# Kernel tuning notes

Measured on AMD Instinct MI355X. Metric: run time of the kernel, lower is better.

The kernel has to match this reference:

```python
import jax, jax.numpy as jnp
import numpy as np

DIM = 1024
HEADS = 16
HEAD_DIM = DIM // HEADS
SCALE = DIM ** -0.5  # note: original uses full dim, not head_dim


def setup_inputs() -> dict:
    key = jax.random.key(0)
    k1, k2, k3, k4 = jax.random.split(key, 4)
    x = jax.random.normal(k1, (4, 2048, DIM), dtype=jnp.float32)
    # nn.Linear(dim, 3*dim, bias=False): weight [3*dim, dim]; y = x @ W.T
    w_qkv = jax.random.normal(k2, (3 * DIM, DIM), dtype=jnp.float32) * (DIM ** -0.5)
    w_out = jax.random.normal(k3, (DIM, DIM), dtype=jnp.float32) * (DIM ** -0.5)
    b_out = jax.random.normal(k4, (DIM,), dtype=jnp.float32) * 0.01
    return {"x": x, "w_qkv": w_qkv, "w_out": w_out, "b_out": b_out}


def reference(x, w_qkv, w_out, b_out):
    b, n, d = x.shape
    qkv = jnp.einsum('bnd,ed->bne', x, w_qkv)  # [b, n, 3*dim]
    # rearrange 'b n (qkv h d) -> qkv b h n d'
    qkv = qkv.reshape(b, n, 3, HEADS, HEAD_DIM).transpose(2, 0, 3, 1, 4)
    q, k, v = qkv[0], qkv[1], qkv[2]
    dots = jnp.einsum('bhid,bhjd->bhij', q, k) * SCALE
    attn = jax.nn.softmax(dots, axis=-1)
    out = jnp.einsum('bhij,bhjd->bhid', attn, v)
    out = out.transpose(0, 2, 1, 3).reshape(b, n, d)  # b h n d -> b n (h d)
    return jnp.einsum('bnd,ed->bne', out, w_out) + b_out
```

## Files before the change

### kernel.cpp

```cpp
#include <hip/hip_runtime.h>
#include <stdint.h>
#include <stddef.h>

typedef _Float16 f16;
typedef __attribute__((ext_vector_type(8))) _Float16 f16x8;
typedef __attribute__((ext_vector_type(4))) _Float16 f16x4;
typedef __attribute__((ext_vector_type(4))) float f32x4;

#define DINL __device__ __forceinline__

DINL void async_cp16(void* lds, const void* gmem) {
    __builtin_amdgcn_global_load_lds(
        (const __attribute__((address_space(1))) void*)(uintptr_t)gmem,
        (__attribute__((address_space(3))) void*)(uint32_t)(uintptr_t)lds,
        16, 0, 0);
}

__global__ void cast_fused(const float* __restrict__ x, f16* __restrict__ xh,
                           const float* __restrict__ wq, f16* __restrict__ wqh,
                           const float* __restrict__ wo, f16* __restrict__ woh,
                           float qs) {
    int stride = gridDim.x * blockDim.x;
    for (int i = blockIdx.x * blockDim.x + threadIdx.x; i < 3145728; i += stride) {
        const float4* src; f16x4* dst; float s = 1.f;
        if (i < 2097152)      { src = (const float4*)x  + i;            dst = (f16x4*)xh  + i; }
        else if (i < 2883584) { int j = i - 2097152; src = (const float4*)wq + j; dst = (f16x4*)wqh + j;
                                if (j < 262144) s = qs; }
        else                  { int j = i - 2883584; src = (const float4*)wo + j; dst = (f16x4*)woh + j; }
        float4 v = *src;
        f16x4 h = { (f16)(v.x * s), (f16)(v.y * s), (f16)(v.z * s), (f16)(v.w * s) };
        *dst = h;
    }
}

template <typename TC, bool HAS_BIAS>
__global__ __launch_bounds__(256) void gemm_bt(
    const f16* __restrict__ A, const f16* __restrict__ B,
    TC* __restrict__ C, const float* __restrict__ bias,
    int M, int N, int K)
{
    constexpr int BK = 64;
    __shared__ __align__(16) f16 As[128 * BK];
    __shared__ __align__(16) f16 Bs[128 * BK];

    const int tid  = threadIdx.x;
    const int lane = tid & 63;
    const int wave = tid >> 6;
    const int bm = blockIdx.y * 128;
    const int bn = blockIdx.x * 128;
    const int wr = (wave >> 1) * 64;
    const int wc = (wave & 1) * 64;

    f32x4 acc[4][4] = {};

    for (int k0 = 0; k0 < K; k0 += BK) {
#pragma unroll
        for (int it = 0; it < 4; ++it) {
            int s = tid + it * 256, row = s >> 3, cc = (s & 7) ^ (row & 7);
            async_cp16(&As[(size_t)s * 8], &A[(size_t)(bm + row) * K + k0 + cc * 8]);
        }
#pragma unroll
        for (int it = 0; it < 4; ++it) {
            int s = tid + it * 256, row = s >> 3, cc = (s & 7) ^ (row & 7);
            async_cp16(&Bs[(size_t)s * 8], &B[(size_t)(bn + row) * K + k0 + cc * 8]);
        }
        __syncthreads();

#pragma unroll
        for (int ks = 0; ks < BK; ks += 32) {
            const int rlo = lane & 15;
            const int c = (ks >> 3) + (lane >> 4);
            f16x8 af[4], bf[4];
#pragma unroll
            for (int m = 0; m < 4; ++m) {
                int r = wr + m * 16 + rlo;
                af[m] = *(const f16x8*)&As[(r * 8 + (c ^ (r & 7))) * 8];
            }
#pragma unroll
            for (int n = 0; n < 4; ++n) {
                int r = wc + n * 16 + rlo;
                bf[n] = *(const f16x8*)&Bs[(r * 8 + (c ^ (r & 7))) * 8];
            }
#pragma unroll
            for (int m = 0; m < 4; ++m)
#pragma unroll
                for (int n = 0; n < 4; ++n)
                    acc[m][n] = __builtin_amdgcn_mfma_f32_16x16x32_f16(af[m], bf[n], acc[m][n], 0, 0, 0);
        }
        __syncthreads();
    }

#pragma unroll
    for (int n = 0; n < 4; ++n) {
        const int gc = bn + wc + n * 16 + (lane & 15);
        float bv = 0.f;
        if constexpr (HAS_BIAS) bv = bias[gc];
#pragma unroll
        for (int m = 0; m < 4; ++m) {
            const int gr0 = bm + wr + m * 16 + ((lane >> 4) << 2);
#pragma unroll
            for (int r = 0; r < 4; ++r) {
                float v = acc[m][n][r] + bv;
                if constexpr (sizeof(TC) == 4) C[(size_t)(gr0 + r) * N + gc] = v;
                else                           C[(size_t)(gr0 + r) * N + gc] = (f16)v;
            }
        }
    }
}

__global__ __launch_bounds__(256) void transpose_v(const f16* __restrict__ qkv, f16* __restrict__ vt) {
    __shared__ float T[64][65];
    const int bid = blockIdx.x, bh = bid >> 5, st = bid & 31;
    const int b = bh >> 4, h = bh & 15, s0 = st * 64;
    const int tid = threadIdx.x;
    const int rs = tid >> 2, c0 = (tid & 3) * 16;
    const f16* src = &qkv[(size_t)(b * 2048 + s0 + rs) * 3072 + 2048 + h * 64 + c0];
    f16x8 v0 = ((const f16x8*)src)[0], v1 = ((const f16x8*)src)[1];
#pragma unroll
    for (int e = 0; e < 8; ++e) { T[rs][c0 + e] = (float)v0[e]; T[rs][c0 + 8 + e] = (float)v1[e]; }
    __syncthreads();
    const int rd = tid >> 2, k0 = (tid & 3) * 16;
    f16x8 w0, w1;
#pragma unroll
    for (int e = 0; e < 8; ++e) { w0[e] = (f16)T[k0 + e][rd]; w1[e] = (f16)T[k0 + 8 + e][rd]; }
    f16* dst = &vt[(size_t)(bh * 64 + rd) * 2048 + s0 + k0];
    ((f16x8*)dst)[0] = w0; ((f16x8*)dst)[1] = w1;
}

DINL void stage_kv(f16* Kd, f16* Vd, const f16* qkv, const f16* vt,
                   size_t base, int bh, int jt, int tid) {
    int s = tid, row = s >> 3, cc = (s & 7) ^ (row & 7);
    int s2 = tid + 256, row2 = s2 >> 3, cc2 = (s2 & 7) ^ (row2 & 7);
    async_cp16(&Kd[s * 8],  &qkv[base + 1024 + (size_t)(jt * 64 + row)  * 3072 + cc * 8]);
    async_cp16(&Kd[s2 * 8], &qkv[base + 1024 + (size_t)(jt * 64 + row2) * 3072 + cc2 * 8]);
    async_cp16(&Vd[s * 8],  &vt[(size_t)(bh * 64 + row)  * 2048 + jt * 64 + cc * 8]);
    async_cp16(&Vd[s2 * 8], &vt[(size_t)(bh * 64 + row2) * 2048 + jt * 64 + cc2 * 8]);
}

__global__ __launch_bounds__(256) void attn_mfma(
    const f16* __restrict__ qkv, const f16* __restrict__ vt, f16* __restrict__ out)
{
    constexpr int TD = 3072;
    __shared__ __align__(16) f16 Qs[64 * 64];
    __shared__ __align__(16) f16 Ks[2][64 * 64];
    __shared__ __align__(16) f16 Vs[2][64 * 64];
    __shared__ __align__(16) f16 Ps[4][16 * 64];

    const int tid = threadIdx.x, lane = tid & 63, wave = tid >> 6;
    const int bh = blockIdx.x, b = bh >> 4, h = bh & 15;
    const int q0 = blockIdx.y * 64;
    const size_t base = (size_t)b * 2048 * TD + h * 64;
    const int lo = lane & 15, hi = lane >> 4;

#pragma unroll
    for (int it = 0; it < 2; ++it) {
        int s = tid + it * 256, row = s >> 3, cc = (s & 7) ^ (row & 7);
        async_cp16(&Qs[s * 8], &qkv[base + (size_t)(q0 + row) * TD + cc * 8]);
    }
    stage_kv(Ks[0], Vs[0], qkv, vt, base, bh, 0, tid);

    float lp[4] = {};
    f32x4 o_[4] = {};

    for (int jt = 0; jt < 32; ++jt) {
        const int cur = jt & 1;
        __syncthreads();
        if (jt + 1 < 32)
            stage_kv(Ks[cur ^ 1], Vs[cur ^ 1], qkv, vt, base, bh, jt + 1, tid);

        f32x4 sc[4] = {};
#pragma unroll
        for (int ks = 0; ks < 2; ++ks) {
            const int c = ks * 4 + hi;
            const int r = wave * 16 + lo;
            f16x8 af = *(const f16x8*)&Qs[(r * 8 + (c ^ (r & 7))) * 8];
#pragma unroll
            for (int n = 0; n < 4; ++n) {
                int key = n * 16 + lo;
                f16x8 bf = *(const f16x8*)&Ks[cur][(key * 8 + (c ^ (key & 7))) * 8];
                sc[n] = __builtin_amdgcn_mfma_f32_16x16x32_f16(af, bf, sc[n], 0, 0, 0);
            }
        }

#pragma unroll
        for (int r = 0; r < 4; ++r) {
            float p0 = exp2f(sc[0][r]), p1 = exp2f(sc[1][r]);
            float p2 = exp2f(sc[2][r]), p3 = exp2f(sc[3][r]);
            lp[r] += (p0 + p1) + (p2 + p3);
            const int row_w = hi * 4 + r;
            const int rw7 = row_w & 7;
            const int ebase = row_w * 64 + (lo & 7);
            float pv[4] = { p0, p1, p2, p3 };
#pragma unroll
            for (int n = 0; n < 4; ++n) {
                int chunk = n * 2 + (lo >> 3);
                Ps[wave][ebase + ((chunk ^ rw7) << 3)] = (f16)pv[n];
            }
        }
        asm volatile("s_waitcnt lgkmcnt(0)" ::: "memory");

#pragma unroll
        for (int ks = 0; ks < 2; ++ks) {
            const int c = ks * 4 + hi;
            const int r = lo;
            f16x8 pa = *(const f16x8*)&Ps[wave][(r * 8 + (c ^ (r & 7))) * 8];
#pragma unroll
            for (int n = 0; n < 4; ++n) {
                int dd = n * 16 + lo;
                f16x8 vb = *(const f16x8*)&Vs[cur][(dd * 8 + (c ^ (dd & 7))) * 8];
                o_[n] = __builtin_amdgcn_mfma_f32_16x16x32_f16(pa, vb, o_[n], 0, 0, 0);
            }
        }
    }

#pragma unroll
    for (int r = 0; r < 4; ++r) {
#pragma unroll
        for (int off = 1; off < 16; off <<= 1)
            lp[r] += __shfl_xor(lp[r], off);
        float inv = 1.f / lp[r];
        int row = q0 + wave * 16 + hi * 4 + r;
#pragma unroll
        for (int n = 0; n < 4; ++n) {
            int dim = h * 64 + n * 16 + lo;
            out[(size_t)(b * 2048 + row) * 1024 + dim] = (f16)(o_[n][r] * inv);
        }
    }
}

extern "C" void kernel_launch(void* const* d_in, const int* in_sizes, int n_in,
                              void* d_out, int out_size, void* d_ws, size_t ws_size,
                              hipStream_t stream)
{
    int ix = 0, iq = 1, iw = 2, ib = 3;
    for (int i = 0; i < n_in; ++i) {
        if      (in_sizes[i] == 8388608) ix = i;
        else if (in_sizes[i] == 3145728) iq = i;
        else if (in_sizes[i] == 1048576) iw = i;
        else if (in_sizes[i] == 1024)    ib = i;
    }
    const float* x     = (const float*)d_in[ix];
    const float* w_qkv = (const float*)d_in[iq];
    const float* w_out = (const float*)d_in[iw];
    const float* b_out = (const float*)d_in[ib];

    char* ws = (char*)d_ws;
    f16* Xh    = (f16*)(ws + 0);
    f16* AOh   = Xh;
    f16* Wqkvh = (f16*)(ws + 16777216);
    f16* QKVh  = (f16*)(ws + 23068672);
    f16* Vth   = (f16*)(ws + 73400320);
    f16* Wouth = (f16*)(ws + 90177536);

    const float QSCALE = 0.03125f * 1.4426950408889634f;

    cast_fused<<<3072, 256, 0, stream>>>(x, Xh, w_qkv, Wqkvh, w_out, Wouth, QSCALE);

    gemm_bt<f16, false><<<dim3(24, 64), 256, 0, stream>>>(
        Xh, Wqkvh, QKVh, nullptr, 8192, 3072, 1024);

    transpose_v<<<2048, 256, 0, stream>>>(QKVh, Vth);

    attn_mfma<<<dim3(64, 32), 256, 0, stream>>>(QKVh, Vth, AOh);

    gemm_bt<float, true><<<dim3(8, 64), 256, 0, stream>>>(
        AOh, Wouth, (float*)d_out, b_out, 8192, 1024, 1024);
}
```

Baseline: 350.2 us.

## Keep Q fragments in registers and compute transposed scores for vectorized P stores

Q fragments are now loaded straight from global memory into registers once per block instead of being staged through LDS and re-read every key tile, which removes the Qs buffer and its per-iteration LDS reads. The QK^T MFMA operands are swapped so each lane holds a column of scores for a single query row. That lets P be written to LDS as packed f16x4 stores with an XOR swizzle, and lets the row sum be kept as one scalar reduced with two shuffles at the end. Launch bounds now request 4 blocks per CU, which may constrain registers; the Q load is synchronous rather than async.

```diff
diff --git a/kernel.cpp b/kernel.cpp
--- a/kernel.cpp
+++ b/kernel.cpp
@@ -137,11 +137,10 @@
     async_cp16(&Vd[s2 * 8], &vt[(size_t)(bh * 64 + row2) * 2048 + jt * 64 + cc2 * 8]);
 }
 
-__global__ __launch_bounds__(256) void attn_mfma(
+__global__ __launch_bounds__(256, 4) void attn_mfma(
     const f16* __restrict__ qkv, const f16* __restrict__ vt, f16* __restrict__ out)
 {
     constexpr int TD = 3072;
-    __shared__ __align__(16) f16 Qs[64 * 64];
     __shared__ __align__(16) f16 Ks[2][64 * 64];
     __shared__ __align__(16) f16 Vs[2][64 * 64];
     __shared__ __align__(16) f16 Ps[4][16 * 64];
@@ -150,17 +149,17 @@
     const int bh = blockIdx.x, b = bh >> 4, h = bh & 15;
     const int q0 = blockIdx.y * 64;
     const size_t base = (size_t)b * 2048 * TD + h * 64;
-    const int lo = lane & 15, hi = lane >> 4;
-
-#pragma unroll
-    for (int it = 0; it < 2; ++it) {
-        int s = tid + it * 256, row = s >> 3, cc = (s & 7) ^ (row & 7);
-        async_cp16(&Qs[s * 8], &qkv[base + (size_t)(q0 + row) * TD + cc * 8]);
-    }
+    const int lo = lane & 15, hi = lane >> 4, ml = lo & 7;
+
+    const f16* qp = &qkv[base + (size_t)(q0 + wave * 16 + lo) * TD + hi * 8];
+    f16x8 qf0 = *(const f16x8*)qp;
+    f16x8 qf1 = *(const f16x8*)(qp + 32);
+
     stage_kv(Ks[0], Vs[0], qkv, vt, base, bh, 0, tid);
 
-    float lp[4] = {};
+    float lsum = 0.f;
     f32x4 o_[4] = {};
+    char* Pb = (char*)&Ps[wave][0];
 
     for (int jt = 0; jt < 32; ++jt) {
         const int cur = jt & 1;
@@ -172,38 +171,29 @@
 #pragma unroll
         for (int ks = 0; ks < 2; ++ks) {
             const int c = ks * 4 + hi;
-            const int r = wave * 16 + lo;
-            f16x8 af = *(const f16x8*)&Qs[(r * 8 + (c ^ (r & 7))) * 8];
+            const f16x8 qf = ks ? qf1 : qf0;
 #pragma unroll
             for (int n = 0; n < 4; ++n) {
                 int key = n * 16 + lo;
-                f16x8 bf = *(const f16x8*)&Ks[cur][(key * 8 + (c ^ (key & 7))) * 8];
-                sc[n] = __builtin_amdgcn_mfma_f32_16x16x32_f16(af, bf, sc[n], 0, 0, 0);
-            }
-        }
-
-#pragma unroll
-        for (int r = 0; r < 4; ++r) {
-            float p0 = exp2f(sc[0][r]), p1 = exp2f(sc[1][r]);
-            float p2 = exp2f(sc[2][r]), p3 = exp2f(sc[3][r]);
-            lp[r] += (p0 + p1) + (p2 + p3);
-            const int row_w = hi * 4 + r;
-            const int rw7 = row_w & 7;
-            const int ebase = row_w * 64 + (lo & 7);
-            float pv[4] = { p0, p1, p2, p3 };
-#pragma unroll
-            for (int n = 0; n < 4; ++n) {
-                int chunk = n * 2 + (lo >> 3);
-                Ps[wave][ebase + ((chunk ^ rw7) << 3)] = (f16)pv[n];
-            }
+                f16x8 kf = *(const f16x8*)&Ks[cur][(key * 8 + (c ^ (key & 7))) * 8];
+                sc[n] = __builtin_amdgcn_mfma_f32_16x16x32_f16(kf, qf, sc[n], 0, 0, 0);
+            }
+        }
+
+#pragma unroll
+        for (int n = 0; n < 4; ++n) {
+            float p0 = exp2f(sc[n][0]), p1 = exp2f(sc[n][1]);
+            float p2 = exp2f(sc[n][2]), p3 = exp2f(sc[n][3]);
+            lsum += (p0 + p1) + (p2 + p3);
+            f16x4 h4 = { (f16)p0, (f16)p1, (f16)p2, (f16)p3 };
+            *(f16x4*)(Pb + ((lo * 128 + hi * 8 + n * 32) ^ (ml << 4))) = h4;
         }
         asm volatile("s_waitcnt lgkmcnt(0)" ::: "memory");
 
 #pragma unroll
         for (int ks = 0; ks < 2; ++ks) {
             const int c = ks * 4 + hi;
-            const int r = lo;
-            f16x8 pa = *(const f16x8*)&Ps[wave][(r * 8 + (c ^ (r & 7))) * 8];
+            f16x8 pa = *(const f16x8*)(Pb + ((lo * 128 + c * 16) ^ (ml << 4)));
 #pragma unroll
             for (int n = 0; n < 4; ++n) {
                 int dd = n * 16 + lo;
@@ -213,12 +203,11 @@
         }
     }
 
+    lsum += __shfl_xor(lsum, 16);
+    lsum += __shfl_xor(lsum, 32);
 #pragma unroll
     for (int r = 0; r < 4; ++r) {
-#pragma unroll
-        for (int off = 1; off < 16; off <<= 1)
-            lp[r] += __shfl_xor(lp[r], off);
-        float inv = 1.f / lp[r];
+        float inv = 1.f / __shfl(lsum, hi * 4 + r);
         int row = q0 + wave * 16 + hi * 4 + r;
 #pragma unroll
         for (int n = 0; n < 4; ++n) {
```

Result: faster. 322.2 us (-8.0%).
